# Kernel optimization log

Measured on AMD Instinct MI355X. Metric: run time of the kernel, lower is better.

The kernel has to match this reference:

```python
import jax, jax.numpy as jnp
import numpy as np

DIM = 64
HEADS = 8
K_RATIOS = [0.5, 0.67, 0.75, 0.8]
BN_EPS = 1e-5


def conv3d(x, w, b, groups=1, pad=0):
    out = jax.lax.conv_general_dilated(
        x, w, window_strides=(1, 1, 1), padding=[(pad, pad)] * 3,
        dimension_numbers=('NCDHW', 'OIDHW', 'NCDHW'),
        feature_group_count=groups)
    return out + b[None, :, None, None, None]


def bn_eval(x, gamma, beta):
    # BatchNorm3d in inference mode with init running stats (mean=0, var=1)
    s = gamma / np.float32(np.sqrt(1.0 + BN_EPS))
    return x * s[None, :, None, None, None] + beta[None, :, None, None, None]


def setup_inputs() -> dict:
    key = jax.random.key(0)
    ks = jax.random.split(key, 12)
    def p(k, shape, scale=0.05):
        return jax.random.normal(k, shape, dtype=jnp.float32) * scale
    B, D, H, W = 2, 16, 64, 64
    return {
        'x': jax.random.normal(ks[0], (B, DIM, D, H, W), dtype=jnp.float32),
        'w_qkv': p(ks[1], (3 * DIM, DIM, 1, 1, 1)),
        'b_qkv': p(ks[2], (3 * DIM,)),
        'w_dw': p(ks[3], (3 * DIM, 1, 3, 3, 3)),
        'b_dw': p(ks[4], (3 * DIM,)),
        'temperature': jnp.ones((HEADS, 1, 1), jnp.float32),
        'attn_weights': jnp.ones((len(K_RATIOS),), jnp.float32),
        'w_recal': p(ks[5], (DIM, DIM, 1, 1, 1)),
        'b_recal': p(ks[6], (DIM,)),
        'bn1_g': jnp.ones((DIM,), jnp.float32),
        'bn1_b': jnp.zeros((DIM,), jnp.float32),
        'w_fus': p(ks[7], (DIM, 2 * DIM, 1, 1, 1)),
        'b_fus': p(ks[8], (DIM,)),
        'bn2_g': jnp.ones((DIM,), jnp.float32),
        'bn2_b': jnp.zeros((DIM,), jnp.float32),
        'w_proj': p(ks[9], (DIM, DIM, 1, 1, 1)),
        'b_proj': p(ks[10], (DIM,)),
    }


def reference(x, w_qkv, b_qkv, w_dw, b_dw, temperature, attn_weights,
              w_recal, b_recal, bn1_g, bn1_b, w_fus, b_fus, bn2_g, bn2_b,
              w_proj, b_proj):
    b, c, d, h, w = x.shape
    residual = x
    qkv = conv3d(conv3d(x, w_qkv, b_qkv), w_dw, b_dw, groups=3 * DIM, pad=1)
    q, k, v = jnp.split(qkv, 3, axis=1)
    def to_heads(t):  # b (head ch) d h w -> b head ch (d h w)
        return t.reshape(b, HEADS, c // HEADS, d * h * w)
    q, k, v = to_heads(q), to_heads(k), to_heads(v)
    # L2-normalize along token dim (torch F.normalize, eps=1e-12)
    q = q / jnp.maximum(jnp.linalg.norm(q, axis=-1, keepdims=True), 1e-12)
    k = k / jnp.maximum(jnp.linalg.norm(k, axis=-1, keepdims=True), 1e-12)
    C = q.shape[2]
    attn = jnp.einsum('bhin,bhjn->bhij', q, k) * temperature[None]  # (b,head,C,C)
    soft_w = jax.nn.softmax(attn_weights)
    weighted = 0.0
    for i, ratio in enumerate(K_RATIOS):
        kv = int(C * ratio)
        idx = jax.lax.top_k(attn, kv)[1]                      # (b,head,C,kv)
        mask = jax.nn.one_hot(idx, C, dtype=attn.dtype).sum(-2) > 0
        probs = jax.nn.softmax(jnp.where(mask, attn, -jnp.inf), axis=-1)
        out = jnp.einsum('bhij,bhjn->bhin', probs, v)          # (b,head,C,N)
        weighted = weighted + soft_w[i] * out.reshape(b, c, d, h, w)
    recalib = jax.nn.sigmoid(bn_eval(conv3d(weighted, w_recal, b_recal), bn1_g, bn1_b))
    enhanced = weighted * recalib
    fused = jnp.concatenate([enhanced, residual], axis=1)
    output = bn_eval(conv3d(fused, w_fus, b_fus), bn2_g, bn2_b)
    output = conv3d(output, w_proj, b_proj)
    return output
```

## Files before the change

### kernel.cpp

```cpp
#include <hip/hip_runtime.h>
#include <math.h>

#define NPOS 65536
#define DD 16
#define HHH 64
#define WWW 64
#define K3CHUNK 64

typedef __attribute__((ext_vector_type(8))) short bf16x8;
typedef __attribute__((ext_vector_type(4))) short s16x4;
typedef __attribute__((ext_vector_type(4))) float f32x4;

static __device__ __forceinline__ short f2bf(float f) {
    union { float f; unsigned u; } v; v.f = f;
    unsigned r = (v.u + 0x7FFFu + ((v.u >> 16) & 1u)) >> 16;
    return (short)r;
}
static __device__ __forceinline__ float bf2f(short s) {
    union { unsigned u; float f; } v; v.u = ((unsigned)(unsigned short)s) << 16;
    return v.f;
}

__global__ void k0_prep(const float* __restrict__ Wq,
                        const float* __restrict__ Wr, const float* __restrict__ Wf,
                        const float* __restrict__ Wp,
                        const float* __restrict__ brec,
                        const float* __restrict__ bn1g, const float* __restrict__ bn1b,
                        const float* __restrict__ bfus,
                        const float* __restrict__ bn2g, const float* __restrict__ bn2b,
                        short* __restrict__ WqA, short* __restrict__ WrA,
                        short* __restrict__ WfA, short* __restrict__ WpA,
                        float* __restrict__ bias1, float* __restrict__ bias2) {
    const float invs = 1.0f / sqrtf(1.0f + 1e-5f);
    int idx = blockIdx.x * 256 + threadIdx.x;
    if (idx < 12288) {
        int e = idx & 7, l = (idx >> 3) & 63, m = (idx >> 9) & 3;
        int t = (idx >> 11) & 1, c = idx >> 12;
        int out = c*64 + 16*m + (l & 15), k = 32*t + ((l >> 4) << 3) + e;
        WqA[idx] = f2bf(Wq[out*64 + k]);
        return;
    }
    int i = idx - 12288;
    if (i < 4096) {
        int e = i & 7, l = (i >> 3) & 63, m = (i >> 9) & 3, t = (i >> 11) & 1;
        int out = 16*m + (l & 15), k = 32*t + ((l >> 4) << 3) + e;
        WrA[i] = f2bf(Wr[out*64 + k] * bn1g[out] * invs);
        return;
    }
    i -= 4096;
    if (i < 8192) {
        int e = i & 7, l = (i >> 3) & 63, m = (i >> 9) & 3, t = (i >> 11) & 3;
        int out = 16*m + (l & 15), k = 32*t + ((l >> 4) << 3) + e;
        WfA[i] = f2bf(Wf[out*128 + k] * bn2g[out] * invs);
        return;
    }
    i -= 8192;
    if (i < 4096) {
        int e = i & 7, l = (i >> 3) & 63, m = (i >> 9) & 3, t = (i >> 11) & 1;
        int out = 16*m + (l & 15), k = 32*t + ((l >> 4) << 3) + e;
        WpA[i] = f2bf(Wp[out*64 + k]);
        return;
    }
    i -= 4096;
    if (i < 64)       bias1[i]    = brec[i]    * bn1g[i]    * invs + bn1b[i];
    else if (i < 128) bias2[i-64] = bfus[i-64] * bn2g[i-64] * invs + bn2b[i-64];
}

__global__ __launch_bounds__(256) void k1_qkv(const float* __restrict__ x,
        const short* __restrict__ WqA, const float* __restrict__ bq,
        short* __restrict__ qkv) {
    __shared__ __align__(16) float Xs[64 * 64];
    __shared__ __align__(16) float As[64 * 64];
    const int tid = threadIdx.x, lane = tid & 63, wv = tid >> 6;
    const int blk = blockIdx.x;
    const int b = blk >> 10, n0 = (blk & 1023) << 6;
    const float* xg = x + ((long long)b * 64) * NPOS + n0;
    #pragma unroll
    for (int kk = 0; kk < 4; ++kk) {
        int idx = tid + kk * 256;
        int ch = idx >> 4, p = (idx & 15) << 2;
        *(float4*)(Xs + ch * 64 + p) = *(const float4*)(xg + (long long)ch * NPOS + p);
    }
    const int bcol  = wv * 16 + (lane & 15);
    const int bk    = (lane >> 4) << 3;
    const int drow0 = (lane >> 4) << 2;
    __syncthreads();

    bf16x8 B0, B1;
    #pragma unroll
    for (int e = 0; e < 8; ++e) B0[e] = f2bf(Xs[(bk + e) * 64 + bcol]);
    #pragma unroll
    for (int e = 0; e < 8; ++e) B1[e] = f2bf(Xs[(32 + bk + e) * 64 + bcol]);

    #pragma unroll
    for (int c = 0; c < 3; ++c) {
        f32x4 D[4];
        #pragma unroll
        for (int m = 0; m < 4; ++m) {
            bf16x8 A0 = *(const bf16x8*)(WqA + (((c * 2 + 0) * 4 + m) * 64 + lane) * 8);
            bf16x8 A1 = *(const bf16x8*)(WqA + (((c * 2 + 1) * 4 + m) * 64 + lane) * 8);
            f32x4 a = {0.f, 0.f, 0.f, 0.f};
            a = __builtin_amdgcn_mfma_f32_16x16x32_bf16(A0, B0, a, 0, 0, 0);
            a = __builtin_amdgcn_mfma_f32_16x16x32_bf16(A1, B1, a, 0, 0, 0);
            float4 bb = *(const float4*)(bq + c * 64 + 16 * m + drow0);
            a[0] += bb.x; a[1] += bb.y; a[2] += bb.z; a[3] += bb.w;
            D[m] = a;
        }
        if (c) __syncthreads();
        #pragma unroll
        for (int m = 0; m < 4; ++m)
            #pragma unroll
            for (int r = 0; r < 4; ++r)
                As[(16 * m + drow0 + r) * 64 + bcol] = D[m][r];
        __syncthreads();
        const int row = tid >> 2, q = tid & 3;
        bf16x8 o0, o1;
        #pragma unroll
        for (int j = 0; j < 8; ++j) {
            o0[j] = f2bf(As[row * 64 + q * 16 + j]);
            o1[j] = f2bf(As[row * 64 + q * 16 + 8 + j]);
        }
        short* op = qkv + ((long long)b * 192 + c * 64 + row) * NPOS + n0 + q * 16;
        *(bf16x8*)(op)     = o0;
        *(bf16x8*)(op + 8) = o1;
    }
}

__global__ __launch_bounds__(256) void k2_dw(const short* __restrict__ qkv,
        const float* __restrict__ Wd, const float* __restrict__ bd,
        short* __restrict__ qkv2) {
    __shared__ __align__(16) float tile[108 * 72];
    __shared__ float wsh[28];
    const int tid = threadIdx.x;
    const int lane = tid & 63;
    const int bc  = blockIdx.x >> 4;
    const int sub = blockIdx.x & 15;
    const int d0  = (sub >> 2) << 2;
    const int h0  = (sub & 3) << 4;
    const int c   = bc % 192;

    if (tid < 27) wsh[tid] = Wd[c * 27 + tid];
    if (tid == 31) wsh[27] = bd[c];

    const short* in = qkv + (long long)bc * NPOS;
    for (int i = tid; i < 864; i += 256) {
        const int r = i >> 3, q8 = i & 7;
        const int dd = r / 18;
        const int hh = r - dd * 18;
        const int d = d0 + dd - 1;
        const int h = h0 + hh - 1;
        float4 f0 = make_float4(0.f, 0.f, 0.f, 0.f);
        float4 f1 = make_float4(0.f, 0.f, 0.f, 0.f);
        if (d >= 0 && d < DD && h >= 0 && h < HHH) {
            bf16x8 raw = *(const bf16x8*)(in + (d << 12) + (h << 6) + (q8 << 3));
            f0 = make_float4(bf2f(raw[0]), bf2f(raw[1]), bf2f(raw[2]), bf2f(raw[3]));
            f1 = make_float4(bf2f(raw[4]), bf2f(raw[5]), bf2f(raw[6]), bf2f(raw[7]));
        }
        *(float4*)(tile + r * 72 + (q8 << 3))     = f0;
        *(float4*)(tile + r * 72 + (q8 << 3) + 4) = f1;
    }
    __syncthreads();

    float wreg[27];
    #pragma unroll
    for (int s = 0; s < 27; ++s) wreg[s] = wsh[s];
    const float bias = wsh[27];

    const int wl = tid & 15;
    const int oh = tid >> 4;
    const int w0 = wl << 2;

    float acc[4][4];
    #pragma unroll
    for (int od = 0; od < 4; ++od)
        #pragma unroll
        for (int j = 0; j < 4; ++j) acc[od][j] = bias;

    #pragma unroll
    for (int kh = 0; kh < 3; ++kh) {
        #pragma unroll
        for (int dp = 0; dp < 6; ++dp) {
            const float* row = tile + (dp * 18 + oh + kh) * 72 + w0;
            const float4 v = *(const float4*)(row);
            float lf = __shfl(v.w, lane - 1, 64);
            float rt = __shfl(v.x, lane + 1, 64);
            lf = (wl == 0)  ? 0.f : lf;
            rt = (wl == 15) ? 0.f : rt;
            const float win[6] = {lf, v.x, v.y, v.z, v.w, rt};
            #pragma unroll
            for (int od = 0; od < 4; ++od) {
                const int kd = dp - od;
                if (kd < 0 || kd > 2) continue;
                const float W0 = wreg[kd * 9 + kh * 3 + 0];
                const float W1 = wreg[kd * 9 + kh * 3 + 1];
                const float W2 = wreg[kd * 9 + kh * 3 + 2];
                #pragma unroll
                for (int j = 0; j < 4; ++j)
                    acc[od][j] = fmaf(W0, win[j],
                                 fmaf(W1, win[j+1], fmaf(W2, win[j+2], acc[od][j])));
            }
        }
    }
    short* outp = qkv2 + (long long)bc * NPOS + (h0 + oh) * 64 + w0;
    #pragma unroll
    for (int od = 0; od < 4; ++od) {
        s16x4 o;
        #pragma unroll
        for (int j = 0; j < 4; ++j) o[j] = f2bf(acc[od][j]);
        *(s16x4*)(outp + ((d0 + od) << 12)) = o;
    }
}

__global__ __launch_bounds__(256) void k3_gram(const short* __restrict__ qkv2,
                                               float* __restrict__ partial) {
    const int blk = blockIdx.x;
    const int chunk = blk & (K3CHUNK - 1);
    const int bh = blk >> 6;
    const int b = bh >> 3, h = bh & 7;
    const int tid = threadIdx.x, lane = tid & 63, wv = tid >> 6;
    const short* base = qkv2 + ((long long)b * 192 + h * 8) * NPOS;
    const int ch = lane & 15;
    const long long roff = (ch < 8 ? (long long)ch : (long long)(56 + ch)) * NPOS;
    const short* p = base + roff + chunk * 1024 + wv * 256 + ((lane >> 4) << 3);

    f32x4 a0 = {0.f, 0.f, 0.f, 0.f}, a1 = {0.f, 0.f, 0.f, 0.f};
    #pragma unroll
    for (int it = 0; it < 4; ++it) {
        bf16x8 f0 = *(const bf16x8*)(p + it * 64);
        bf16x8 f1 = *(const bf16x8*)(p + it * 64 + 32);
        a0 = __builtin_amdgcn_mfma_f32_16x16x32_bf16(f0, f0, a0, 0, 0, 0);
        a1 = __builtin_amdgcn_mfma_f32_16x16x32_bf16(f1, f1, a1, 0, 0, 0);
    }
    __shared__ float gs[4][256];
    #pragma unroll
    for (int r = 0; r < 4; ++r)
        gs[wv][(((lane >> 4) << 2) + r) * 16 + (lane & 15)] = a0[r] + a1[r];
    __syncthreads();
    const int row = tid >> 4, col = tid & 15;
    float v = gs[0][tid] + gs[1][tid] + gs[2][tid] + gs[3][tid];
    float* pp = partial + ((long long)bh * K3CHUNK + chunk) * 80;
    if (row < 8 && col >= 8)      pp[row * 8 + (col - 8)] = v;
    else if (row == col && row < 8) pp[64 + row] = v;
    else if (row == col)            pp[72 + row - 8] = v;
}

__global__ void k3b_reduce(const float* __restrict__ partial, float* __restrict__ gram) {
    int s = blockIdx.x * 256 + threadIdx.x;
    if (s >= 16 * 80) return;
    int bh = s / 80, slot = s % 80;
    float acc = 0.f;
    for (int c = 0; c < K3CHUNK; ++c)
        acc += partial[((long long)bh * K3CHUNK + c) * 80 + slot];
    gram[s] = acc;
}

__global__ void k4_combine(const float* __restrict__ gram, const float* __restrict__ temp,
                           const float* __restrict__ aw, float* __restrict__ P) {
    int t = threadIdx.x;
    if (t >= 128) return;
    int bh = t >> 3, i = t & 7;
    int h = bh & 7;
    const float* g = gram + bh * 80;
    float qn = fmaxf(sqrtf(g[64 + i]), 1e-12f);
    float tp = temp[h];
    float attn[8];
    #pragma unroll
    for (int j = 0; j < 8; ++j) {
        float kn = fmaxf(sqrtf(g[72 + j]), 1e-12f);
        attn[j] = g[i * 8 + j] / (qn * kn) * tp;
    }
    float awv[4];
    float am = -3.4e38f;
    for (int r = 0; r < 4; ++r) { awv[r] = aw[r]; am = fmaxf(am, awv[r]); }
    float asum = 0.f;
    for (int r = 0; r < 4; ++r) { awv[r] = expf(awv[r] - am); asum += awv[r]; }
    const int kvs[4] = {4, 5, 6, 6};
    float Pacc[8];
    #pragma unroll
    for (int j = 0; j < 8; ++j) Pacc[j] = 0.f;
    for (int r = 0; r < 4; ++r) {
        float sw = awv[r] / asum;
        int kv = kvs[r];
        bool sel[8];
        #pragma unroll
        for (int j = 0; j < 8; ++j) sel[j] = false;
        for (int m = 0; m < kv; ++m) {
            int best = 0; float bv = -3.4e38f;
            for (int j = 0; j < 8; ++j)
                if (!sel[j] && attn[j] > bv) { bv = attn[j]; best = j; }
            sel[best] = true;
        }
        float mx = -3.4e38f;
        for (int j = 0; j < 8; ++j) if (sel[j]) mx = fmaxf(mx, attn[j]);
        float es = 0.f, e[8];
        for (int j = 0; j < 8; ++j) { e[j] = sel[j] ? expf(attn[j] - mx) : 0.f; es += e[j]; }
        for (int j = 0; j < 8; ++j) Pacc[j] += sw * e[j] / es;
    }
    for (int j = 0; j < 8; ++j) P[t * 8 + j] = Pacc[j];
}

__global__ void k4b_pfrag(const float* __restrict__ P, short* __restrict__ PA) {
    int idx = blockIdx.x * 256 + threadIdx.x;
    int e = idx & 7, l = (idx >> 3) & 63, m = (idx >> 9) & 3;
    int t = (idx >> 11) & 1, b = idx >> 12;
    int out = 16*m + (l & 15), k = 32*t + ((l >> 4) << 3) + e;
    float v = ((k >> 3) == (out >> 3)) ? P[(b * 64 + out) * 8 + (k & 7)] : 0.f;
    PA[idx] = f2bf(v);
}

__global__ __launch_bounds__(256) void k5_tail(
        const short* __restrict__ qkv2, const float* __restrict__ x,
        const short* __restrict__ PA, const short* __restrict__ WrA,
        const short* __restrict__ WfA, const short* __restrict__ WpA,
        const float* __restrict__ bias1, const float* __restrict__ bias2,
        const float* __restrict__ bp, float* __restrict__ out) {
    __shared__ __align__(16) float As[64 * 64];
    __shared__ __align__(16) float Xs[64 * 64];
    const int tid = threadIdx.x, lane = tid & 63, wv = tid >> 6;
    const int blk = blockIdx.x;
    const int b = blk >> 10, n0 = (blk & 1023) << 6;
    const short* vg = qkv2 + ((long long)b * 192 + 128) * NPOS + n0;
    const float* xg = x + ((long long)b * 64) * NPOS + n0;
    #pragma unroll
    for (int kk = 0; kk < 4; ++kk) {
        int idx = tid + kk * 256;
        int ch = idx >> 4, p = (idx & 15) << 2;
        *(float4*)(Xs + ch * 64 + p) = *(const float4*)(xg + (long long)ch * NPOS + p);
    }
    #pragma unroll
    for (int kk = 0; kk < 2; ++kk) {
        int i = tid + kk * 256;
        int ch = i >> 3, p0 = (i & 7) << 3;
        bf16x8 raw = *(const bf16x8*)(vg + (long long)ch * NPOS + p0);
        *(float4*)(As + ch * 64 + p0) =
            make_float4(bf2f(raw[0]), bf2f(raw[1]), bf2f(raw[2]), bf2f(raw[3]));
        *(float4*)(As + ch * 64 + p0 + 4) =
            make_float4(bf2f(raw[4]), bf2f(raw[5]), bf2f(raw[6]), bf2f(raw[7]));
    }
    bf16x8 pA[2][4];
    #pragma unroll
    for (int t = 0; t < 2; ++t)
        #pragma unroll
        for (int m = 0; m < 4; ++m)
            pA[t][m] = *(const bf16x8*)(PA + (((b * 2 + t) * 4 + m) * 64 + lane) * 8);
    const int bcol  = wv * 16 + (lane & 15);
    const int bk    = (lane >> 4) << 3;
    const int drow0 = (lane >> 4) << 2;
    __syncthreads();

    auto loadB = [&](const float* S, int kbase) {
        bf16x8 r;
        #pragma unroll
        for (int e = 0; e < 8; ++e) r[e] = f2bf(S[(kbase + bk + e) * 64 + bcol]);
        return r;
    };

    f32x4 Dw[4];
    {
        bf16x8 B0 = loadB(As, 0), B1 = loadB(As, 32);
        #pragma unroll
        for (int m = 0; m < 4; ++m) {
            f32x4 a = {0.f, 0.f, 0.f, 0.f};
            a = __builtin_amdgcn_mfma_f32_16x16x32_bf16(pA[0][m], B0, a, 0, 0, 0);
            a = __builtin_amdgcn_mfma_f32_16x16x32_bf16(pA[1][m], B1, a, 0, 0, 0);
            Dw[m] = a;
        }
    }
    __syncthreads();
    #pragma unroll
    for (int m = 0; m < 4; ++m)
        #pragma unroll
        for (int r = 0; r < 4; ++r)
            As[(16 * m + drow0 + r) * 64 + bcol] = Dw[m][r];
    __syncthreads();

    float enh[4][4];
    {
        bf16x8 rA[2][4];
        #pragma unroll
        for (int t = 0; t < 2; ++t)
            #pragma unroll
            for (int m = 0; m < 4; ++m)
                rA[t][m] = *(const bf16x8*)(WrA + ((t * 4 + m) * 64 + lane) * 8);
        bf16x8 B0 = loadB(As, 0), B1 = loadB(As, 32);
        #pragma unroll
        for (int m = 0; m < 4; ++m) {
            f32x4 a = {0.f, 0.f, 0.f, 0.f};
            a = __builtin_amdgcn_mfma_f32_16x16x32_bf16(rA[0][m], B0, a, 0, 0, 0);
            a = __builtin_amdgcn_mfma_f32_16x16x32_bf16(rA[1][m], B1, a, 0, 0, 0);
            #pragma unroll
            for (int r = 0; r < 4; ++r) {
                float z = a[r] + bias1[16 * m + drow0 + r];
                enh[m][r] = Dw[m][r] / (1.f + expf(-z));
            }
        }
    }
    __syncthreads();
    #pragma unroll
    for (int m = 0; m < 4; ++m)
        #pragma unroll
        for (int r = 0; r < 4; ++r)
            As[(16 * m + drow0 + r) * 64 + bcol] = enh[m][r];
    __syncthreads();

    f32x4 D3[4];
    {
        bf16x8 fA[4][4];
        #pragma unroll
        for (int t = 0; t < 4; ++t)
            #pragma unroll
            for (int m = 0; m < 4; ++m)
                fA[t][m] = *(const bf16x8*)(WfA + ((t * 4 + m) * 64 + lane) * 8);
        bf16x8 B0 = loadB(As, 0), B1 = loadB(As, 32);
        bf16x8 B2 = loadB(Xs, 0), B3 = loadB(Xs, 32);
        #pragma unroll
        for (int m = 0; m < 4; ++m) {
            f32x4 a = {0.f, 0.f, 0.f, 0.f};
            a = __builtin_amdgcn_mfma_f32_16x16x32_bf16(fA[0][m], B0, a, 0, 0, 0);
            a = __builtin_amdgcn_mfma_f32_16x16x32_bf16(fA[1][m], B1, a, 0, 0, 0);
            a = __builtin_amdgcn_mfma_f32_16x16x32_bf16(fA[2][m], B2, a, 0, 0, 0);
            a = __builtin_amdgcn_mfma_f32_16x16x32_bf16(fA[3][m], B3, a, 0, 0, 0);
            #pragma unroll
            for (int r = 0; r < 4; ++r) a[r] += bias2[16 * m + drow0 + r];
            D3[m] = a;
        }
    }
    __syncthreads();
    #pragma unroll
    for (int m = 0; m < 4; ++m)
        #pragma unroll
        for (int r = 0; r < 4; ++r)
            As[(16 * m + drow0 + r) * 64 + bcol] = D3[m][r];
    __syncthreads();

    f32x4 D4[4];
    {
        bf16x8 qA[2][4];
        #pragma unroll
        for (int t = 0; t < 2; ++t)
            #pragma unroll
            for (int m = 0; m < 4; ++m)
                qA[t][m] = *(const bf16x8*)(WpA + ((t * 4 + m) * 64 + lane) * 8);
        bf16x8 B0 = loadB(As, 0), B1 = loadB(As, 32);
        #pragma unroll
        for (int m = 0; m < 4; ++m) {
            f32x4 a = {0.f, 0.f, 0.f, 0.f};
            a = __builtin_amdgcn_mfma_f32_16x16x32_bf16(qA[0][m], B0, a, 0, 0, 0);
            a = __builtin_amdgcn_mfma_f32_16x16x32_bf16(qA[1][m], B1, a, 0, 0, 0);
            #pragma unroll
            for (int r = 0; r < 4; ++r) a[r] += bp[16 * m + drow0 + r];
            D4[m] = a;
        }
    }
    __syncthreads();
    #pragma unroll
    for (int m = 0; m < 4; ++m)
        #pragma unroll
        for (int r = 0; r < 4; ++r)
            As[(16 * m + drow0 + r) * 64 + bcol] = D4[m][r];
    __syncthreads();
    const int row = tid >> 2, q = tid & 3;
    #pragma unroll
    for (int j = 0; j < 4; ++j) {
        int p = q * 4 + j * 16;
        *(float4*)(out + ((long long)b * 64 + row) * NPOS + n0 + p) =
            *(const float4*)(As + row * 64 + p);
    }
}

extern "C" void kernel_launch(void* const* d_in, const int* in_sizes, int n_in,
                              void* d_out, int out_size, void* d_ws, size_t ws_size,
                              hipStream_t stream) {
    (void)in_sizes; (void)n_in; (void)out_size; (void)ws_size;
    const float* x     = (const float*)d_in[0];
    const float* w_qkv = (const float*)d_in[1];
    const float* b_qkv = (const float*)d_in[2];
    const float* w_dw  = (const float*)d_in[3];
    const float* b_dw  = (const float*)d_in[4];
    const float* temp  = (const float*)d_in[5];
    const float* aw    = (const float*)d_in[6];
    const float* w_rec = (const float*)d_in[7];
    const float* b_rec = (const float*)d_in[8];
    const float* bn1g  = (const float*)d_in[9];
    const float* bn1b  = (const float*)d_in[10];
    const float* w_fus = (const float*)d_in[11];
    const float* b_fus = (const float*)d_in[12];
    const float* bn2g  = (const float*)d_in[13];
    const float* bn2b  = (const float*)d_in[14];
    const float* w_prj = (const float*)d_in[15];
    const float* b_prj = (const float*)d_in[16];
    float* out = (float*)d_out;

    short* qkv  = (short*)d_ws;
    short* qkv2 = qkv + 25165824;
    float* part = (float*)(qkv2 + 25165824);
    float* gram = part + 163840;
    float* P    = gram + 1280;
    float* bias1 = P + 1024;
    float* bias2 = bias1 + 64;
    short* WqA  = (short*)(bias2 + 64);
    short* WrA  = WqA + 12288;
    short* WfA  = WrA + 4096;
    short* WpA  = WfA + 8192;
    short* PAb  = WpA + 4096;

    k0_prep<<<113, 256, 0, stream>>>(w_qkv, w_rec, w_fus, w_prj, b_rec, bn1g, bn1b,
                                     b_fus, bn2g, bn2b, WqA, WrA, WfA, WpA, bias1, bias2);
    k1_qkv<<<2048, 256, 0, stream>>>(x, WqA, b_qkv, qkv);
    k2_dw<<<6144, 256, 0, stream>>>(qkv, w_dw, b_dw, qkv2);
    k3_gram<<<16 * K3CHUNK, 256, 0, stream>>>(qkv2, part);
    k3b_reduce<<<5, 256, 0, stream>>>(part, gram);
    k4_combine<<<1, 128, 0, stream>>>(gram, temp, aw, P);
    k4b_pfrag<<<32, 256, 0, stream>>>(P, PAb);
    k5_tail<<<2048, 256, 0, stream>>>(qkv2, x, PAb, WrA, WfA, WpA,
                                      bias1, bias2, b_prj, out);
}
```

Measured before the change: 113.8 us.

## Stream depthwise conv along depth with rolling accumulators, drop LDS tile

The depthwise 3x3x3 conv kernel no longer stages a halo tile in shared memory. Each thread now walks all 16 depth planes, loading its three h-rows straight from global memory and keeping three rolling accumulators, so each output plane is written once all its contributions are in. Blocks drop from 6144 to 1536 and the depth-halo reloads and LDS traffic go away. In exchange, parallelism is lower, each thread has a longer serial loop, and h-halo rows are still re-read from global or cache by neighbouring threads.

```diff
diff --git a/kernel.cpp b/kernel.cpp
--- a/kernel.cpp
+++ b/kernel.cpp
@@ -18,6 +18,10 @@
 }
 static __device__ __forceinline__ float bf2f(short s) {
     union { unsigned u; float f; } v; v.u = ((unsigned)(unsigned short)s) << 16;
+    return v.f;
+}
+static __device__ __forceinline__ float u2f(unsigned u) {
+    union { unsigned u; float f; } v; v.u = u;
     return v.f;
 }
 
@@ -129,36 +133,13 @@
 __global__ __launch_bounds__(256) void k2_dw(const short* __restrict__ qkv,
         const float* __restrict__ Wd, const float* __restrict__ bd,
         short* __restrict__ qkv2) {
-    __shared__ __align__(16) float tile[108 * 72];
     __shared__ float wsh[28];
-    const int tid = threadIdx.x;
-    const int lane = tid & 63;
-    const int bc  = blockIdx.x >> 4;
-    const int sub = blockIdx.x & 15;
-    const int d0  = (sub >> 2) << 2;
-    const int h0  = (sub & 3) << 4;
+    const int tid = threadIdx.x, lane = tid & 63;
+    const int bc  = blockIdx.x >> 2;
+    const int h0  = (blockIdx.x & 3) << 4;
     const int c   = bc % 192;
-
     if (tid < 27) wsh[tid] = Wd[c * 27 + tid];
     if (tid == 31) wsh[27] = bd[c];
-
-    const short* in = qkv + (long long)bc * NPOS;
-    for (int i = tid; i < 864; i += 256) {
-        const int r = i >> 3, q8 = i & 7;
-        const int dd = r / 18;
-        const int hh = r - dd * 18;
-        const int d = d0 + dd - 1;
-        const int h = h0 + hh - 1;
-        float4 f0 = make_float4(0.f, 0.f, 0.f, 0.f);
-        float4 f1 = make_float4(0.f, 0.f, 0.f, 0.f);
-        if (d >= 0 && d < DD && h >= 0 && h < HHH) {
-            bf16x8 raw = *(const bf16x8*)(in + (d << 12) + (h << 6) + (q8 << 3));
-            f0 = make_float4(bf2f(raw[0]), bf2f(raw[1]), bf2f(raw[2]), bf2f(raw[3]));
-            f1 = make_float4(bf2f(raw[4]), bf2f(raw[5]), bf2f(raw[6]), bf2f(raw[7]));
-        }
-        *(float4*)(tile + r * 72 + (q8 << 3))     = f0;
-        *(float4*)(tile + r * 72 + (q8 << 3) + 4) = f1;
-    }
     __syncthreads();
 
     float wreg[27];
@@ -168,46 +149,70 @@
 
     const int wl = tid & 15;
     const int oh = tid >> 4;
+    const int h  = h0 + oh;
     const int w0 = wl << 2;
-
-    float acc[4][4];
-    #pragma unroll
-    for (int od = 0; od < 4; ++od)
-        #pragma unroll
-        for (int j = 0; j < 4; ++j) acc[od][j] = bias;
-
-    #pragma unroll
-    for (int kh = 0; kh < 3; ++kh) {
-        #pragma unroll
-        for (int dp = 0; dp < 6; ++dp) {
-            const float* row = tile + (dp * 18 + oh + kh) * 72 + w0;
-            const float4 v = *(const float4*)(row);
-            float lf = __shfl(v.w, lane - 1, 64);
-            float rt = __shfl(v.x, lane + 1, 64);
+    const short* in = qkv + (long long)bc * NPOS;
+    short* outp = qkv2 + (long long)bc * NPOS + h * 64 + w0;
+
+    float acc[3][4];
+    #pragma unroll
+    for (int j = 0; j < 4; ++j) acc[0][j] = bias;
+
+    #pragma unroll
+    for (int p = 0; p < 16; ++p) {
+        float win[3][6];
+        #pragma unroll
+        for (int kh = 0; kh < 3; ++kh) {
+            const int hh = h + kh - 1;
+            uint2 raw = make_uint2(0u, 0u);
+            if (hh >= 0 && hh < HHH)
+                raw = *(const uint2*)(in + (p << 12) + hh * 64 + w0);
+            const float e0 = u2f(raw.x << 16);
+            const float e1 = u2f(raw.x & 0xffff0000u);
+            const float e2 = u2f(raw.y << 16);
+            const float e3 = u2f(raw.y & 0xffff0000u);
+            float lf = __shfl(e3, (lane + 63) & 63, 64);
+            float rt = __shfl(e0, (lane + 1) & 63, 64);
             lf = (wl == 0)  ? 0.f : lf;
             rt = (wl == 15) ? 0.f : rt;
-            const float win[6] = {lf, v.x, v.y, v.z, v.w, rt};
-            #pragma unroll
-            for (int od = 0; od < 4; ++od) {
-                const int kd = dp - od;
-                if (kd < 0 || kd > 2) continue;
-                const float W0 = wreg[kd * 9 + kh * 3 + 0];
-                const float W1 = wreg[kd * 9 + kh * 3 + 1];
-                const float W2 = wreg[kd * 9 + kh * 3 + 2];
+            win[kh][0] = lf; win[kh][1] = e0; win[kh][2] = e1;
+            win[kh][3] = e2; win[kh][4] = e3; win[kh][5] = rt;
+        }
+        if (p < 15) {
+            const int s = (p + 1) % 3;
+            #pragma unroll
+            for (int j = 0; j < 4; ++j) acc[s][j] = bias;
+        }
+        #pragma unroll
+        for (int dd = 0; dd < 3; ++dd) {
+            const int od = p + 1 - dd;
+            if (od < 0 || od > 15) continue;
+            const int s = od % 3;
+            #pragma unroll
+            for (int kh = 0; kh < 3; ++kh) {
+                const float W0 = wreg[dd * 9 + kh * 3 + 0];
+                const float W1 = wreg[dd * 9 + kh * 3 + 1];
+                const float W2 = wreg[dd * 9 + kh * 3 + 2];
                 #pragma unroll
                 for (int j = 0; j < 4; ++j)
-                    acc[od][j] = fmaf(W0, win[j],
-                                 fmaf(W1, win[j+1], fmaf(W2, win[j+2], acc[od][j])));
+                    acc[s][j] = fmaf(W0, win[kh][j],
+                               fmaf(W1, win[kh][j + 1],
+                               fmaf(W2, win[kh][j + 2], acc[s][j])));
             }
         }
-    }
-    short* outp = qkv2 + (long long)bc * NPOS + (h0 + oh) * 64 + w0;
-    #pragma unroll
-    for (int od = 0; od < 4; ++od) {
+        if (p >= 1) {
+            const int s = (p - 1) % 3;
+            s16x4 o;
+            #pragma unroll
+            for (int j = 0; j < 4; ++j) o[j] = f2bf(acc[s][j]);
+            *(s16x4*)(outp + ((p - 1) << 12)) = o;
+        }
+    }
+    {
         s16x4 o;
         #pragma unroll
-        for (int j = 0; j < 4; ++j) o[j] = f2bf(acc[od][j]);
-        *(s16x4*)(outp + ((d0 + od) << 12)) = o;
+        for (int j = 0; j < 4; ++j) o[j] = f2bf(acc[15 % 3][j]);
+        *(s16x4*)(outp + (15 << 12)) = o;
     }
 }
 
@@ -507,7 +512,7 @@
     k0_prep<<<113, 256, 0, stream>>>(w_qkv, w_rec, w_fus, w_prj, b_rec, bn1g, bn1b,
                                      b_fus, bn2g, bn2b, WqA, WrA, WfA, WpA, bias1, bias2);
     k1_qkv<<<2048, 256, 0, stream>>>(x, WqA, b_qkv, qkv);
-    k2_dw<<<6144, 256, 0, stream>>>(qkv, w_dw, b_dw, qkv2);
+    k2_dw<<<1536, 256, 0, stream>>>(qkv, w_dw, b_dw, qkv2);
     k3_gram<<<16 * K3CHUNK, 256, 0, stream>>>(qkv2, part);
     k3b_reduce<<<5, 256, 0, stream>>>(part, gram);
     k4_combine<<<1, 128, 0, stream>>>(gram, temp, aw, P);
```

New measurement: 119.8 us. +5.3%, slower.
